# Kernel tuning notes

Measured on AMD Instinct MI355X. Metric: run time of the kernel, lower is better.

Reference implementation:

```python
import jax, jax.numpy as jnp
import numpy as np

NEG = -9e15

def _gat_layer(x, adj, W, a_src, a_dst):
    # x: [B,N,Fin], W: [Fin,Fout], a_src/a_dst: [Fout], adj: [N,N]
    h = jnp.einsum('bnf,fo->bno', x, W)                    # [B,N,Fout]
    e_src = jnp.einsum('bno,o->bn', h, a_src)              # [B,N]
    e_dst = jnp.einsum('bno,o->bn', h, a_dst)              # [B,N]
    e = jax.nn.leaky_relu(e_src[:, :, None] + e_dst[:, None, :], 0.2)  # [B,N,N]
    att = jax.nn.softmax(jnp.where(adj > 0, e, NEG), axis=-1)
    return jnp.einsum('bij,bjo->bio', att, h)              # [B,N,Fout]

def setup_inputs() -> dict:
    key = jax.random.key(0)
    ks = jax.random.split(key, 12)
    B, N, Fin = 8, 2048, 128
    H = [128, 128, 64]
    C = 128
    s = lambda *d: 1.0 / np.sqrt(d[0])
    inp = {
        'x':   jax.random.normal(ks[0], (B, N, Fin), jnp.float32),
        'adj': jax.random.normal(ks[1], (N, N), jnp.float32),
        'W1':  jax.random.normal(ks[2], (Fin, H[0]), jnp.float32) * s(Fin),
        'a1s': jax.random.normal(ks[3], (H[0],), jnp.float32) * s(H[0]),
        'a1d': jax.random.normal(ks[4], (H[0],), jnp.float32) * s(H[0]),
        'W2':  jax.random.normal(ks[5], (H[0], H[1]), jnp.float32) * s(H[0]),
        'a2s': jax.random.normal(ks[6], (H[1],), jnp.float32) * s(H[1]),
        'a2d': jax.random.normal(ks[7], (H[1],), jnp.float32) * s(H[1]),
        'W3':  jax.random.normal(ks[8], (H[1], H[2]), jnp.float32) * s(H[1]),
        'a3s': jax.random.normal(ks[9], (H[2],), jnp.float32) * s(H[2]),
        'a3d': jax.random.normal(ks[10], (H[2],), jnp.float32) * s(H[2]),
        'Wlin': jax.random.normal(ks[11], (H[2] * N, C), jnp.float32) * s(H[2] * N),
        'blin': jnp.zeros((C,), jnp.float32),
    }
    return inp

def reference(x, adj, W1, a1s, a1d, W2, a2s, a2d, W3, a3s, a3d, Wlin, blin):
    out = jax.nn.relu(_gat_layer(x, adj, W1, a1s, a1d))
    out = jax.nn.relu(_gat_layer(out, adj, W2, a2s, a2d))
    out = jax.nn.relu(_gat_layer(out, adj, W3, a3s, a3d))
    B = out.shape[0]
    out = out.reshape(B, -1)              # flatten [B, N*H3]
    return out @ Wlin + blin              # [B, num_classes]
```

## Files before the change

kernel.cpp:

```cpp
#include <hip/hip_runtime.h>
#include <stdint.h>


typedef unsigned short u16;
typedef __bf16 bf16x8 __attribute__((ext_vector_type(8)));
typedef float f32x4 __attribute__((ext_vector_type(4)));
typedef u16 u16x8 __attribute__((ext_vector_type(8)));

#define LOG2E 1.44269504088896340736f

__device__ __forceinline__ float b2f(u16 u) {
    union { unsigned int i; float f; } v; v.i = ((unsigned int)u) << 16; return v.f;
}
__device__ __forceinline__ u16 f2b(float f) {
    union { float f; unsigned int i; } v; v.f = f;
    unsigned int i = v.i;
    return (u16)((i + 0x7fffu + ((i >> 16) & 1u)) >> 16);
}
__device__ __forceinline__ float fast_exp2(float x) {
#if __has_builtin(__builtin_amdgcn_exp2f)
    return __builtin_amdgcn_exp2f(x);
#else
    return exp2f(x);
#endif
}

union ABfrag { bf16x8 v; u16x8 u; };

__device__ __forceinline__ void gload_lds16(const u16* g, u16* l) {
    __builtin_amdgcn_global_load_lds((const __attribute__((address_space(1))) void*)g,
                                     (__attribute__((address_space(3))) void*)l,
                                     16, 0, 0);
}

template <int N>
__device__ __forceinline__ void wait_vmcnt() {
    asm volatile("s_waitcnt vmcnt(%0)" :: "i"(N) : "memory");
}
__device__ __forceinline__ void pipe_barrier() {
    __builtin_amdgcn_s_barrier();
    asm volatile("" ::: "memory");
}

__global__ void __launch_bounds__(256) k_mask(const float* __restrict__ adj,
                                              uint32_t* __restrict__ adjm) {
    const int w = threadIdx.x >> 6, lane = threadIdx.x & 63;
    const int row = blockIdx.x * 4 + w;
    const float* ar = adj + (size_t)row * 2048;
    uint32_t* mr = adjm + (size_t)row * 64;
    for (int j0 = 0; j0 < 2048; j0 += 64) {
        unsigned long long m = __ballot(ar[j0 + lane] > 0.f);
        if (lane == 0) {
            mr[(j0 >> 5)] = (uint32_t)m;
            mr[(j0 >> 5) + 1] = (uint32_t)(m >> 32);
        }
    }
}

__global__ void k_prep(const float* __restrict__ W1, const float* __restrict__ W2,
                       const float* __restrict__ W3,
                       const float* __restrict__ a1s, const float* __restrict__ a1d,
                       const float* __restrict__ a2s, const float* __restrict__ a2d,
                       const float* __restrict__ a3s, const float* __restrict__ a3d,
                       u16* __restrict__ Wt1, u16* __restrict__ Wt2, u16* __restrict__ Wt3,
                       float* __restrict__ u1s, float* __restrict__ u1d,
                       float* __restrict__ u2s, float* __restrict__ u2d,
                       float* __restrict__ u3s, float* __restrict__ u3d) {
    if (blockIdx.x == 160) {
        int f = threadIdx.x;
        if (f < 128) {
            float s1 = 0.f, d1 = 0.f, s2 = 0.f, d2 = 0.f, s3 = 0.f, d3 = 0.f;
            for (int o = 0; o < 128; ++o) { float w = W1[f * 128 + o]; s1 += w * a1s[o]; d1 += w * a1d[o]; }
            for (int o = 0; o < 128; ++o) { float w = W2[f * 128 + o]; s2 += w * a2s[o]; d2 += w * a2d[o]; }
            for (int o = 0; o <  64; ++o) { float w = W3[f *  64 + o]; s3 += w * a3s[o]; d3 += w * a3d[o]; }
            u1s[f] = s1 * LOG2E; u1d[f] = d1 * LOG2E;
            u2s[f] = s2 * LOG2E; u2d[f] = d2 * LOG2E;
            u3s[f] = s3 * LOG2E; u3d[f] = d3 * LOG2E;
        }
        return;
    }
    int idx = blockIdx.x * 256 + threadIdx.x;
    if (idx < 16384) {
        int f = idx >> 7, o = idx & 127;
        Wt1[o * 128 + f] = f2b(W1[idx]);
    } else if (idx < 32768) {
        int j = idx - 16384; int f = j >> 7, o = j & 127;
        Wt2[o * 128 + f] = f2b(W2[j]);
    } else if (idx < 40960) {
        int j = idx - 32768; int f = j >> 6, o = j & 63;
        Wt3[o * 128 + f] = f2b(W3[j]);
    }
}

template <int F, bool XF32>
__global__ void __launch_bounds__(256) k_h(const void* __restrict__ xv,
                                           const u16* __restrict__ Wt,
                                           const float* __restrict__ us,
                                           const float* __restrict__ ud,
                                           u16* __restrict__ h_t,
                                           float* __restrict__ esf,
                                           float* __restrict__ edf) {
    constexpr int NT = F / 16;
    constexpr int TNP = 72;
    __shared__ __align__(16) u16 hl[F * TNP];

    const int b = blockIdx.x;
    const int nblk = blockIdx.y;
    const int tid = threadIdx.x;
    const int w = tid >> 6, lane = tid & 63;
    const int quad = lane >> 4, l15 = lane & 15;
    const int n0w = nblk * 64 + w * 16;
    const int i_a = n0w + l15;

    ABfrag afr[4];
    float ps = 0.f, pd = 0.f;
    if (XF32) {
        const float* xr = (const float*)xv + ((size_t)(b * 2048 + i_a)) * 128;
#pragma unroll
        for (int kk = 0; kk < 4; ++kk) {
            const int o8 = kk * 32 + quad * 8;
            float4 x0 = *reinterpret_cast<const float4*>(xr + o8);
            float4 x1 = *reinterpret_cast<const float4*>(xr + o8 + 4);
            float4 s0 = *reinterpret_cast<const float4*>(us + o8);
            float4 s1 = *reinterpret_cast<const float4*>(us + o8 + 4);
            float4 d0 = *reinterpret_cast<const float4*>(ud + o8);
            float4 d1 = *reinterpret_cast<const float4*>(ud + o8 + 4);
            ps += x0.x * s0.x + x0.y * s0.y + x0.z * s0.z + x0.w * s0.w
                + x1.x * s1.x + x1.y * s1.y + x1.z * s1.z + x1.w * s1.w;
            pd += x0.x * d0.x + x0.y * d0.y + x0.z * d0.z + x0.w * d0.w
                + x1.x * d1.x + x1.y * d1.y + x1.z * d1.z + x1.w * d1.w;
            afr[kk].u[0] = f2b(x0.x); afr[kk].u[1] = f2b(x0.y);
            afr[kk].u[2] = f2b(x0.z); afr[kk].u[3] = f2b(x0.w);
            afr[kk].u[4] = f2b(x1.x); afr[kk].u[5] = f2b(x1.y);
            afr[kk].u[6] = f2b(x1.z); afr[kk].u[7] = f2b(x1.w);
        }
    } else {
        const u16* xr = (const u16*)xv + ((size_t)(b * 2048 + i_a)) * 128;
#pragma unroll
        for (int kk = 0; kk < 4; ++kk) {
            const int o8 = kk * 32 + quad * 8;
            u16x8 xa = *reinterpret_cast<const u16x8*>(xr + o8);
            afr[kk].u = xa;
            float4 s0 = *reinterpret_cast<const float4*>(us + o8);
            float4 s1 = *reinterpret_cast<const float4*>(us + o8 + 4);
            float4 d0 = *reinterpret_cast<const float4*>(ud + o8);
            float4 d1 = *reinterpret_cast<const float4*>(ud + o8 + 4);
            float xf[8];
#pragma unroll
            for (int j = 0; j < 8; ++j) xf[j] = b2f(xa[j]);
            ps += xf[0] * s0.x + xf[1] * s0.y + xf[2] * s0.z + xf[3] * s0.w
                + xf[4] * s1.x + xf[5] * s1.y + xf[6] * s1.z + xf[7] * s1.w;
            pd += xf[0] * d0.x + xf[1] * d0.y + xf[2] * d0.z + xf[3] * d0.w
                + xf[4] * d1.x + xf[5] * d1.y + xf[6] * d1.z + xf[7] * d1.w;
        }
    }
    ps += __shfl_xor(ps, 16, 64); ps += __shfl_xor(ps, 32, 64);
    pd += __shfl_xor(pd, 16, 64); pd += __shfl_xor(pd, 32, 64);
    if (quad == 0) {
        const size_t idx = (size_t)(b * 2048 + i_a) * 2;
        float2 sv; sv.x = fast_exp2(ps); sv.y = fast_exp2(0.2f * ps);
        float2 dv; dv.x = fast_exp2(pd); dv.y = fast_exp2(0.2f * pd);
        *reinterpret_cast<float2*>(esf + idx) = sv;
        *reinterpret_cast<float2*>(edf + idx) = dv;
    }

    f32x4 acc[NT];
#pragma unroll
    for (int nt = 0; nt < NT; ++nt) acc[nt] = (f32x4){0.f, 0.f, 0.f, 0.f};
#pragma unroll
    for (int kk = 0; kk < 4; ++kk) {
#pragma unroll
        for (int nt = 0; nt < NT; ++nt) {
            bf16x8 bfv = *reinterpret_cast<const bf16x8*>(
                Wt + (nt * 16 + l15) * 128 + kk * 32 + quad * 8);
            acc[nt] = __builtin_amdgcn_mfma_f32_16x16x32_bf16(afr[kk].v, bfv, acc[nt], 0, 0, 0);
        }
    }

#pragma unroll
    for (int nt = 0; nt < NT; ++nt)
#pragma unroll
        for (int r = 0; r < 4; ++r)
            hl[(nt * 16 + l15) * TNP + w * 16 + quad * 4 + r] = f2b(acc[nt][r]);
    __syncthreads();
    if (tid < F * 2) {
        int o = tid >> 1, half = tid & 1;
        const u16* src = hl + o * TNP + half * 32;
        u16* dst = h_t + ((size_t)(b * F + o)) * 2048 + nblk * 64 + half * 32;
#pragma unroll
        for (int c = 0; c < 4; ++c)
            *reinterpret_cast<u16x8*>(dst + c * 8) =
                *reinterpret_cast<const u16x8*>(src + c * 8);
    }
}

template <int F, bool OUT_F32>
__global__ void __launch_bounds__(512) k_attn(const float* __restrict__ esf,
                                              const float* __restrict__ edf,
                                              const uint32_t* __restrict__ adjm,
                                              const u16* __restrict__ h_t,
                                              void* __restrict__ outp) {
    constexpr int NT = F / 16;
    constexpr int G  = F / 32;
    __shared__ __align__(16) u16 Ht[2][3][F * 64];
    __shared__ __align__(16) float eL[4096];
    __shared__ __align__(16) uint32_t mL[64 * 64];
    float* accLDS = (float*)&Ht[0][0][0];

    const int b = blockIdx.x;
    const int iblk = blockIdx.y;
    const int tid = threadIdx.x;
    const int grp = tid >> 8;
    const int t8 = tid & 255;
    const int w = t8 >> 6;
    const int lane = tid & 63;
    const int quad = lane >> 4, l15 = lane & 15;
    const int i_a = iblk * 64 + w * 16 + l15;
    const int r_loc = w * 16 + l15;

    const float2 esp = *reinterpret_cast<const float2*>(esf + ((size_t)(b * 2048 + i_a)) * 2);
    const float Es = esp.x, Fs = esp.y;
    const u16* hb = h_t + (size_t)b * F * 2048;

    const int lro = lane >> 3;
    const int lcp = lane & 7;
    const int jt0 = grp * 16;

    ABfrag onesf;
#pragma unroll
    for (int j = 0; j < 8; ++j) onesf.u[j] = 0x3F80;

    f32x4 acc[NT];
#pragma unroll
    for (int nt = 0; nt < NT; ++nt) acc[nt] = (f32x4){0.f, 0.f, 0.f, 0.f};
    f32x4 dccc = (f32x4){0.f, 0.f, 0.f, 0.f};

    {
        const float4* esrc = (const float4*)(edf + (size_t)b * 4096);
        float4* edst = (float4*)eL;
#pragma unroll
        for (int t = 0; t < 2; ++t) edst[tid + t * 512] = esrc[tid + t * 512];
        const uint2* msrc = (const uint2*)(adjm + (size_t)(iblk * 64) * 64);
#pragma unroll
        for (int t = 0; t < 4; ++t) {
            int idx = tid + t * 512;
            int r = idx >> 5, k = idx & 31;
            uint2 v = msrc[idx];
            *reinterpret_cast<uint2*>((char*)mL + r * 256 + ((k ^ (r & 31)) * 8)) = v;
        }
    }

    auto STAGE = [&](int jt, int slot) {
        const int j0 = jt * 64;
        u16* lbase = &Ht[grp][slot][0];
#pragma unroll
        for (int it = 0; it < G; ++it) {
            int ro = (it * 4 + w) * 8 + lro;
            int c = lcp ^ (ro & 7);
            gload_lds16(hb + (size_t)ro * 2048 + j0 + c * 8, lbase + (it * 4 + w) * 512);
        }
    };

    f32x4 ec[8]; uint2 mc;
    auto loadE = [&](int jt, f32x4* e, uint2& m) {
        const float* eb = eL + (size_t)(jt * 64 + quad * 8) * 2;
#pragma unroll
        for (int q = 0; q < 4; ++q) e[q] = *reinterpret_cast<const f32x4*>(eb + q * 4);
#pragma unroll
        for (int q = 0; q < 4; ++q) e[4 + q] = *reinterpret_cast<const f32x4*>(eb + 64 + q * 4);
        m = *reinterpret_cast<const uint2*>((const char*)mL + r_loc * 256 + ((jt ^ (r_loc & 31)) * 8));
    };

    auto compute = [&](int slot) {
        ABfrag af[2];
#pragma unroll
        for (int kk = 0; kk < 2; ++kk) {
            const uint32_t word = kk ? mc.y : mc.x;
#pragma unroll
            for (int px = 0; px < 4; ++px) {
                const f32x4 q = ec[kk * 4 + px];
                float w0 = fmaxf(Es * q.x, Fs * q.y);
                float w1 = fmaxf(Es * q.z, Fs * q.w);
                const uint32_t s0 = 0u - ((word >> (quad * 8 + px * 2)) & 1u);
                const uint32_t s1 = 0u - ((word >> (quad * 8 + px * 2 + 1)) & 1u);
                w0 = __uint_as_float(__float_as_uint(w0) & s0);
                w1 = __uint_as_float(__float_as_uint(w1) & s1);
                af[kk].v[px * 2]     = (__bf16)w0;
                af[kk].v[px * 2 + 1] = (__bf16)w1;
            }
        }
        const u16* tb = &Ht[grp][slot][0];
        __builtin_amdgcn_s_setprio(1);
#pragma unroll
        for (int kk = 0; kk < 2; ++kk) {
#pragma unroll
            for (int nt = 0; nt < NT; ++nt) {
                int ob = nt * 16 + l15;
                int c = kk * 4 + quad;
                bf16x8 bfv = *reinterpret_cast<const bf16x8*>(
                    tb + ob * 64 + ((c ^ (ob & 7)) * 8));
                acc[nt] = __builtin_amdgcn_mfma_f32_16x16x32_bf16(af[kk].v, bfv, acc[nt], 0, 0, 0);
            }
            dccc = __builtin_amdgcn_mfma_f32_16x16x32_bf16(af[kk].v, onesf.v, dccc, 0, 0, 0);
        }
        __builtin_amdgcn_s_setprio(0);
    };

    __syncthreads();
    loadE(jt0, ec, mc);
    STAGE(jt0, 0);
    STAGE(jt0 + 1, 1);

    int sc = 0, sp = 2;
    for (int jj = 0; jj < 15; ++jj) {
        wait_vmcnt<G>();
        pipe_barrier();
        if (jj < 14) STAGE(jt0 + jj + 2, sp);
        f32x4 en[8]; uint2 mn;
        loadE(jt0 + jj + 1, en, mn);
        compute(sc);
#pragma unroll
        for (int q = 0; q < 8; ++q) ec[q] = en[q];
        mc = mn;
        sc = (sc == 2) ? 0 : sc + 1;
        sp = (sp == 2) ? 0 : sp + 1;
    }
    wait_vmcnt<0>();
    pipe_barrier();
    compute(sc);

    __syncthreads();
    if (grp == 1) {
#pragma unroll
        for (int nt = 0; nt < NT; ++nt)
            *reinterpret_cast<f32x4*>(&accLDS[(t8 * (NT + 1) + nt) * 4]) = acc[nt];
        *reinterpret_cast<f32x4*>(&accLDS[(t8 * (NT + 1) + NT) * 4]) = dccc;
    }
    __syncthreads();
    if (grp == 0) {
#pragma unroll
        for (int nt = 0; nt < NT; ++nt)
            acc[nt] += *reinterpret_cast<const f32x4*>(&accLDS[(t8 * (NT + 1) + nt) * 4]);
        dccc += *reinterpret_cast<const f32x4*>(&accLDS[(t8 * (NT + 1) + NT) * 4]);
        float dinv[4];
#pragma unroll
        for (int r = 0; r < 4; ++r)
            dinv[r] = 1.0f / fmaxf(dccc[r], 1e-30f);
        const int ib = iblk * 64 + w * 16 + quad * 4;
        if (OUT_F32) {
            float* o3 = (float*)outp;
#pragma unroll
            for (int nt = 0; nt < NT; ++nt)
#pragma unroll
                for (int r = 0; r < 4; ++r) {
                    float vv = fmaxf(acc[nt][r] * dinv[r], 0.f);
                    o3[((size_t)(b * 2048 + ib + r)) * F + nt * 16 + l15] = vv;
                }
        } else {
            u16* xo = (u16*)outp;
#pragma unroll
            for (int nt = 0; nt < NT; ++nt)
#pragma unroll
                for (int r = 0; r < 4; ++r) {
                    float vv = fmaxf(acc[nt][r] * dinv[r], 0.f);
                    xo[((size_t)(b * 2048 + ib + r)) * F + nt * 16 + l15] = f2b(vv);
                }
        }
    }
}

__global__ void __launch_bounds__(256) k_lin(const float* __restrict__ o3,
                                             const float* __restrict__ Wlin,
                                             float* __restrict__ pbuf) {
    __shared__ float xc[8][256];
    __shared__ float red[8][8][128];
    const int tid = threadIdx.x;
    const int k0 = blockIdx.x * 256;
    for (int idx = tid; idx < 2048; idx += 256) {
        int bb = idx >> 8, kk = idx & 255;
        xc[bb][kk] = o3[(size_t)bb * 131072 + k0 + kk];
    }
    __syncthreads();
    const int o4 = tid & 31;
    const int kb = tid >> 5;
    f32x4 acc[8];
#pragma unroll
    for (int bb = 0; bb < 8; ++bb) acc[bb] = (f32x4){0.f, 0.f, 0.f, 0.f};
    const float* wp = Wlin + (size_t)(k0 + kb * 32) * 128 + o4 * 4;
#pragma unroll 4
    for (int k = 0; k < 32; ++k) {
        f32x4 wv = *reinterpret_cast<const f32x4*>(wp + (size_t)k * 128);
#pragma unroll
        for (int bb = 0; bb < 8; ++bb) acc[bb] += wv * xc[bb][kb * 32 + k];
    }
#pragma unroll
    for (int bb = 0; bb < 8; ++bb)
        *reinterpret_cast<f32x4*>(&red[kb][bb][o4 * 4]) = acc[bb];
    __syncthreads();
    const int f = tid * 4;
    const int bb = f >> 7, o = f & 127;
    f32x4 s = (f32x4){0.f, 0.f, 0.f, 0.f};
#pragma unroll
    for (int k2 = 0; k2 < 8; ++k2) s += *reinterpret_cast<const f32x4*>(&red[k2][bb][o]);
    *reinterpret_cast<f32x4*>(&pbuf[(size_t)blockIdx.x * 1024 + f]) = s;
}

__global__ void __launch_bounds__(256) k_bias(const float* __restrict__ pbuf,
                                              const float* __restrict__ blin,
                                              float* __restrict__ out) {
    __shared__ float red[256];
    const int tid = threadIdx.x;
    const int p16 = tid >> 4;
    const int fo = tid & 15;
    const int f0 = blockIdx.x * 16;
    float s = 0.f;
#pragma unroll 4
    for (int p = p16; p < 512; p += 16)
        s += pbuf[(size_t)p * 1024 + f0 + fo];
    red[tid] = s;
    __syncthreads();
    if (tid < 16) {
        float t = 0.f;
#pragma unroll
        for (int k = 0; k < 16; ++k) t += red[k * 16 + tid];
        out[f0 + tid] = t + blin[(f0 + tid) & 127];
    }
}

extern "C" void kernel_launch(void* const* d_in, const int* in_sizes, int n_in,
                              void* d_out, int out_size, void* d_ws, size_t ws_size,
                              hipStream_t stream) {
    (void)in_sizes; (void)n_in; (void)out_size;
    const float* x    = (const float*)d_in[0];
    const float* adj  = (const float*)d_in[1];
    const float* W1   = (const float*)d_in[2];
    const float* a1s  = (const float*)d_in[3];
    const float* a1d  = (const float*)d_in[4];
    const float* W2   = (const float*)d_in[5];
    const float* a2s  = (const float*)d_in[6];
    const float* a2d  = (const float*)d_in[7];
    const float* W3   = (const float*)d_in[8];
    const float* a3s  = (const float*)d_in[9];
    const float* a3d  = (const float*)d_in[10];
    const float* Wlin = (const float*)d_in[11];
    const float* blin = (const float*)d_in[12];

    char* ws = (char*)d_ws;
    u16*   h_t = (u16*)ws;
    size_t off = (size_t)4 << 20;
    float* esf = (float*)(ws + off); off += 131072;
    float* edf = (float*)(ws + off); off += 131072;
    u16*   Wt1 = (u16*)(ws + off);   off += 32768;
    u16*   Wt2 = (u16*)(ws + off);   off += 32768;
    u16*   Wt3 = (u16*)(ws + off);   off += 16384;
    float* u1s = (float*)(ws + off); off += 512;
    float* u1d = (float*)(ws + off); off += 512;
    float* u2s = (float*)(ws + off); off += 512;
    float* u2d = (float*)(ws + off); off += 512;
    float* u3s = (float*)(ws + off); off += 512;
    float* u3d = (float*)(ws + off); off += 512;
    uint32_t* adjm = (uint32_t*)(ws + off); off += 524288;
    float* pbuf = (float*)(ws + off); off += (size_t)512 * 1024 * 4;
    u16* actA;
    if (ws_size >= off + ((size_t)4 << 20)) {
        actA = (u16*)(ws + off);
    } else {
        actA = (u16*)d_in[0];
    }
    float* o3 = (float*)actA;

    dim3 g(8, 32);
    k_mask<<<512, 256, 0, stream>>>(adj, adjm);
    k_prep<<<161, 256, 0, stream>>>(W1, W2, W3, a1s, a1d, a2s, a2d, a3s, a3d,
                                    Wt1, Wt2, Wt3, u1s, u1d, u2s, u2d, u3s, u3d);

    k_h<128, true ><<<g, 256, 0, stream>>>((const void*)x, Wt1, u1s, u1d, h_t, esf, edf);
    k_attn<128, false><<<g, 512, 0, stream>>>(esf, edf, adjm, h_t, (void*)actA);

    k_h<128, false><<<g, 256, 0, stream>>>((const void*)actA, Wt2, u2s, u2d, h_t, esf, edf);
    k_attn<128, false><<<g, 512, 0, stream>>>(esf, edf, adjm, h_t, (void*)actA);

    k_h<64, false><<<g, 256, 0, stream>>>((const void*)actA, Wt3, u3s, u3d, h_t, esf, edf);
    k_attn<64, true ><<<g, 512, 0, stream>>>(esf, edf, adjm, h_t, (void*)o3);

    k_lin<<<512, 256, 0, stream>>>(o3, Wlin, pbuf);
    k_bias<<<64, 256, 0, stream>>>(pbuf, blin, (float*)d_out);
}
```

Measured before the change: 240.4 us.

## Halve attention block to 256 threads with two row tiles per wave; split k_h output columns

k_attn now runs 256 threads per block, and each wave computes two 16-row tiles that share every staged H fragment read from LDS. This doubles MFMA work per B-fragment load and cuts the number of waves per block. The E/mask prefetch is also simplified to load just before compute instead of being double-buffered. Separately, k_h is split over two grid blocks per row tile, each computing half of the output features, which doubles the grid so more CUs are busy. The costs are higher register pressure in k_attn, fewer waves available to hide latency, and x being reloaded twice in k_h.

Result: slower. 253.6 us (+5.5%).

```diff
diff --git a/kernel.cpp b/kernel.cpp
--- a/kernel.cpp
+++ b/kernel.cpp
@@ -100,12 +100,13 @@
                                            u16* __restrict__ h_t,
                                            float* __restrict__ esf,
                                            float* __restrict__ edf) {
-    constexpr int NT = F / 16;
+    constexpr int NTB = F / 32;
     constexpr int TNP = 72;
-    __shared__ __align__(16) u16 hl[F * TNP];
+    __shared__ __align__(16) u16 hl[(F / 2) * TNP];
 
     const int b = blockIdx.x;
-    const int nblk = blockIdx.y;
+    const int nb2 = blockIdx.y;
+    const int nblk = nb2 >> 1, ohalf = nb2 & 1;
     const int tid = threadIdx.x;
     const int w = tid >> 6, lane = tid & 63;
     const int quad = lane >> 4, l15 = lane & 15;
@@ -154,39 +155,42 @@
                 + xf[4] * d1.x + xf[5] * d1.y + xf[6] * d1.z + xf[7] * d1.w;
         }
     }
-    ps += __shfl_xor(ps, 16, 64); ps += __shfl_xor(ps, 32, 64);
-    pd += __shfl_xor(pd, 16, 64); pd += __shfl_xor(pd, 32, 64);
-    if (quad == 0) {
-        const size_t idx = (size_t)(b * 2048 + i_a) * 2;
-        float2 sv; sv.x = fast_exp2(ps); sv.y = fast_exp2(0.2f * ps);
-        float2 dv; dv.x = fast_exp2(pd); dv.y = fast_exp2(0.2f * pd);
-        *reinterpret_cast<float2*>(esf + idx) = sv;
-        *reinterpret_cast<float2*>(edf + idx) = dv;
-    }
-
-    f32x4 acc[NT];
-#pragma unroll
-    for (int nt = 0; nt < NT; ++nt) acc[nt] = (f32x4){0.f, 0.f, 0.f, 0.f};
+    if (ohalf == 0) {
+        ps += __shfl_xor(ps, 16, 64); ps += __shfl_xor(ps, 32, 64);
+        pd += __shfl_xor(pd, 16, 64); pd += __shfl_xor(pd, 32, 64);
+        if (quad == 0) {
+            const size_t idx = (size_t)(b * 2048 + i_a) * 2;
+            float2 sv; sv.x = fast_exp2(ps); sv.y = fast_exp2(0.2f * ps);
+            float2 dv; dv.x = fast_exp2(pd); dv.y = fast_exp2(0.2f * pd);
+            *reinterpret_cast<float2*>(esf + idx) = sv;
+            *reinterpret_cast<float2*>(edf + idx) = dv;
+        }
+    }
+
+    f32x4 acc[NTB];
+#pragma unroll
+    for (int nt = 0; nt < NTB; ++nt) acc[nt] = (f32x4){0.f, 0.f, 0.f, 0.f};
 #pragma unroll
     for (int kk = 0; kk < 4; ++kk) {
 #pragma unroll
-        for (int nt = 0; nt < NT; ++nt) {
+        for (int nt = 0; nt < NTB; ++nt) {
             bf16x8 bfv = *reinterpret_cast<const bf16x8*>(
-                Wt + (nt * 16 + l15) * 128 + kk * 32 + quad * 8);
+                Wt + (ohalf * (F / 2) + nt * 16 + l15) * 128 + kk * 32 + quad * 8);
             acc[nt] = __builtin_amdgcn_mfma_f32_16x16x32_bf16(afr[kk].v, bfv, acc[nt], 0, 0, 0);
         }
     }
 
 #pragma unroll
-    for (int nt = 0; nt < NT; ++nt)
+    for (int nt = 0; nt < NTB; ++nt)
 #pragma unroll
         for (int r = 0; r < 4; ++r)
             hl[(nt * 16 + l15) * TNP + w * 16 + quad * 4 + r] = f2b(acc[nt][r]);
     __syncthreads();
-    if (tid < F * 2) {
-        int o = tid >> 1, half = tid & 1;
-        const u16* src = hl + o * TNP + half * 32;
-        u16* dst = h_t + ((size_t)(b * F + o)) * 2048 + nblk * 64 + half * 32;
+    if (tid < F) {
+        int o_loc = tid >> 1, half32 = tid & 1;
+        const u16* src = hl + o_loc * TNP + half32 * 32;
+        u16* dst = h_t + ((size_t)(b * F + ohalf * (F / 2) + o_loc)) * 2048
+                   + nblk * 64 + half32 * 32;
 #pragma unroll
         for (int c = 0; c < 4; ++c)
             *reinterpret_cast<u16x8*>(dst + c * 8) =
@@ -195,13 +199,13 @@
 }
 
 template <int F, bool OUT_F32>
-__global__ void __launch_bounds__(512) k_attn(const float* __restrict__ esf,
+__global__ void __launch_bounds__(256) k_attn(const float* __restrict__ esf,
                                               const float* __restrict__ edf,
                                               const uint32_t* __restrict__ adjm,
                                               const u16* __restrict__ h_t,
                                               void* __restrict__ outp) {
     constexpr int NT = F / 16;
-    constexpr int G  = F / 32;
+    constexpr int G  = F / 16;
     __shared__ __align__(16) u16 Ht[2][3][F * 64];
     __shared__ __align__(16) float eL[4096];
     __shared__ __align__(16) uint32_t mL[64 * 64];
@@ -210,16 +214,17 @@
     const int b = blockIdx.x;
     const int iblk = blockIdx.y;
     const int tid = threadIdx.x;
-    const int grp = tid >> 8;
-    const int t8 = tid & 255;
-    const int w = t8 >> 6;
+    const int grp = tid >> 7;
+    const int t128 = tid & 127;
+    const int w = t128 >> 6;
     const int lane = tid & 63;
     const int quad = lane >> 4, l15 = lane & 15;
-    const int i_a = iblk * 64 + w * 16 + l15;
-    const int r_loc = w * 16 + l15;
-
-    const float2 esp = *reinterpret_cast<const float2*>(esf + ((size_t)(b * 2048 + i_a)) * 2);
-    const float Es = esp.x, Fs = esp.y;
+    const int r0 = w * 32 + l15;
+    const int r1 = r0 + 16;
+
+    const float2 e0 = *reinterpret_cast<const float2*>(esf + ((size_t)(b * 2048 + iblk * 64 + r0)) * 2);
+    const float2 e1 = *reinterpret_cast<const float2*>(esf + ((size_t)(b * 2048 + iblk * 64 + r1)) * 2);
+    const float Es0 = e0.x, Fs0 = e0.y, Es1 = e1.x, Fs1 = e1.y;
     const u16* hb = h_t + (size_t)b * F * 2048;
 
     const int lro = lane >> 3;
@@ -230,20 +235,24 @@
 #pragma unroll
     for (int j = 0; j < 8; ++j) onesf.u[j] = 0x3F80;
 
-    f32x4 acc[NT];
-#pragma unroll
-    for (int nt = 0; nt < NT; ++nt) acc[nt] = (f32x4){0.f, 0.f, 0.f, 0.f};
-    f32x4 dccc = (f32x4){0.f, 0.f, 0.f, 0.f};
+    f32x4 acc0[NT], acc1[NT];
+#pragma unroll
+    for (int nt = 0; nt < NT; ++nt) {
+        acc0[nt] = (f32x4){0.f, 0.f, 0.f, 0.f};
+        acc1[nt] = (f32x4){0.f, 0.f, 0.f, 0.f};
+    }
+    f32x4 d0 = (f32x4){0.f, 0.f, 0.f, 0.f};
+    f32x4 d1 = (f32x4){0.f, 0.f, 0.f, 0.f};
 
     {
         const float4* esrc = (const float4*)(edf + (size_t)b * 4096);
         float4* edst = (float4*)eL;
 #pragma unroll
-        for (int t = 0; t < 2; ++t) edst[tid + t * 512] = esrc[tid + t * 512];
+        for (int t = 0; t < 4; ++t) edst[tid + t * 256] = esrc[tid + t * 256];
         const uint2* msrc = (const uint2*)(adjm + (size_t)(iblk * 64) * 64);
 #pragma unroll
-        for (int t = 0; t < 4; ++t) {
-            int idx = tid + t * 512;
+        for (int t = 0; t < 8; ++t) {
+            int idx = tid + t * 256;
             int r = idx >> 5, k = idx & 31;
             uint2 v = msrc[idx];
             *reinterpret_cast<uint2*>((char*)mL + r * 256 + ((k ^ (r & 31)) * 8)) = v;
@@ -255,38 +264,50 @@
         u16* lbase = &Ht[grp][slot][0];
 #pragma unroll
         for (int it = 0; it < G; ++it) {
-            int ro = (it * 4 + w) * 8 + lro;
+            int ci = it * 2 + w;
+            int ro = ci * 8 + lro;
             int c = lcp ^ (ro & 7);
-            gload_lds16(hb + (size_t)ro * 2048 + j0 + c * 8, lbase + (it * 4 + w) * 512);
+            gload_lds16(hb + (size_t)ro * 2048 + j0 + c * 8, lbase + ci * 512);
         }
     };
 
-    f32x4 ec[8]; uint2 mc;
-    auto loadE = [&](int jt, f32x4* e, uint2& m) {
+    f32x4 ec[8]; uint2 mc0, mc1;
+    auto loadE = [&](int jt) {
         const float* eb = eL + (size_t)(jt * 64 + quad * 8) * 2;
 #pragma unroll
-        for (int q = 0; q < 4; ++q) e[q] = *reinterpret_cast<const f32x4*>(eb + q * 4);
-#pragma unroll
-        for (int q = 0; q < 4; ++q) e[4 + q] = *reinterpret_cast<const f32x4*>(eb + 64 + q * 4);
-        m = *reinterpret_cast<const uint2*>((const char*)mL + r_loc * 256 + ((jt ^ (r_loc & 31)) * 8));
+        for (int q = 0; q < 4; ++q) ec[q] = *reinterpret_cast<const f32x4*>(eb + q * 4);
+#pragma unroll
+        for (int q = 0; q < 4; ++q) ec[4 + q] = *reinterpret_cast<const f32x4*>(eb + 64 + q * 4);
+        mc0 = *reinterpret_cast<const uint2*>((const char*)mL + r0 * 256 + ((jt ^ (r0 & 31)) * 8));
+        mc1 = *reinterpret_cast<const uint2*>((const char*)mL + r1 * 256 + ((jt ^ (r1 & 31)) * 8));
     };
 
     auto compute = [&](int slot) {
-        ABfrag af[2];
+        ABfrag af0[2], af1[2];
 #pragma unroll
         for (int kk = 0; kk < 2; ++kk) {
-            const uint32_t word = kk ? mc.y : mc.x;
+            const uint32_t word0 = kk ? mc0.y : mc0.x;
+            const uint32_t word1 = kk ? mc1.y : mc1.x;
 #pragma unroll
             for (int px = 0; px < 4; ++px) {
                 const f32x4 q = ec[kk * 4 + px];
-                float w0 = fmaxf(Es * q.x, Fs * q.y);
-                float w1 = fmaxf(Es * q.z, Fs * q.w);
-                const uint32_t s0 = 0u - ((word >> (quad * 8 + px * 2)) & 1u);
-                const uint32_t s1 = 0u - ((word >> (quad * 8 + px * 2 + 1)) & 1u);
-                w0 = __uint_as_float(__float_as_uint(w0) & s0);
-                w1 = __uint_as_float(__float_as_uint(w1) & s1);
-                af[kk].v[px * 2]     = (__bf16)w0;
-                af[kk].v[px * 2 + 1] = (__bf16)w1;
+                const int bsh = quad * 8 + px * 2;
+                float wa0 = fmaxf(Es0 * q.x, Fs0 * q.y);
+                float wb0 = fmaxf(Es0 * q.z, Fs0 * q.w);
+                float wa1 = fmaxf(Es1 * q.x, Fs1 * q.y);
+                float wb1 = fmaxf(Es1 * q.z, Fs1 * q.w);
+                const uint32_t sa0 = 0u - ((word0 >> bsh) & 1u);
+                const uint32_t sb0 = 0u - ((word0 >> (bsh + 1)) & 1u);
+                const uint32_t sa1 = 0u - ((word1 >> bsh) & 1u);
+                const uint32_t sb1 = 0u - ((word1 >> (bsh + 1)) & 1u);
+                wa0 = __uint_as_float(__float_as_uint(wa0) & sa0);
+                wb0 = __uint_as_float(__float_as_uint(wb0) & sb0);
+                wa1 = __uint_as_float(__float_as_uint(wa1) & sa1);
+                wb1 = __uint_as_float(__float_as_uint(wb1) & sb1);
+                af0[kk].v[px * 2]     = (__bf16)wa0;
+                af0[kk].v[px * 2 + 1] = (__bf16)wb0;
+                af1[kk].v[px * 2]     = (__bf16)wa1;
+                af1[kk].v[px * 2 + 1] = (__bf16)wb1;
             }
         }
         const u16* tb = &Ht[grp][slot][0];
@@ -299,15 +320,16 @@
                 int c = kk * 4 + quad;
                 bf16x8 bfv = *reinterpret_cast<const bf16x8*>(
                     tb + ob * 64 + ((c ^ (ob & 7)) * 8));
-                acc[nt] = __builtin_amdgcn_mfma_f32_16x16x32_bf16(af[kk].v, bfv, acc[nt], 0, 0, 0);
+                acc0[nt] = __builtin_amdgcn_mfma_f32_16x16x32_bf16(af0[kk].v, bfv, acc0[nt], 0, 0, 0);
+                acc1[nt] = __builtin_amdgcn_mfma_f32_16x16x32_bf16(af1[kk].v, bfv, acc1[nt], 0, 0, 0);
             }
-            dccc = __builtin_amdgcn_mfma_f32_16x16x32_bf16(af[kk].v, onesf.v, dccc, 0, 0, 0);
+            d0 = __builtin_amdgcn_mfma_f32_16x16x32_bf16(af0[kk].v, onesf.v, d0, 0, 0, 0);
+            d1 = __builtin_amdgcn_mfma_f32_16x16x32_bf16(af1[kk].v, onesf.v, d1, 0, 0, 0);
         }
         __builtin_amdgcn_s_setprio(0);
     };
 
     __syncthreads();
-    loadE(jt0, ec, mc);
     STAGE(jt0, 0);
     STAGE(jt0 + 1, 1);
 
@@ -316,45 +338,49 @@
         wait_vmcnt<G>();
         pipe_barrier();
         if (jj < 14) STAGE(jt0 + jj + 2, sp);
-        f32x4 en[8]; uint2 mn;
-        loadE(jt0 + jj + 1, en, mn);
+        loadE(jt0 + jj);
         compute(sc);
-#pragma unroll
-        for (int q = 0; q < 8; ++q) ec[q] = en[q];
-        mc = mn;
         sc = (sc == 2) ? 0 : sc + 1;
         sp = (sp == 2) ? 0 : sp + 1;
     }
     wait_vmcnt<0>();
     pipe_barrier();
+    loadE(jt0 + 15);
     compute(sc);
 
     __syncthreads();
     if (grp == 1) {
-#pragma unroll
-        for (int nt = 0; nt < NT; ++nt)
-            *reinterpret_cast<f32x4*>(&accLDS[(t8 * (NT + 1) + nt) * 4]) = acc[nt];
-        *reinterpret_cast<f32x4*>(&accLDS[(t8 * (NT + 1) + NT) * 4]) = dccc;
+        f32x4* basep = reinterpret_cast<f32x4*>(&accLDS[(size_t)t128 * (2 * NT + 2) * 4]);
+#pragma unroll
+        for (int nt = 0; nt < NT; ++nt) { basep[nt] = acc0[nt]; basep[NT + nt] = acc1[nt]; }
+        basep[2 * NT] = d0;
+        basep[2 * NT + 1] = d1;
     }
     __syncthreads();
     if (grp == 0) {
-#pragma unroll
-        for (int nt = 0; nt < NT; ++nt)
-            acc[nt] += *reinterpret_cast<const f32x4*>(&accLDS[(t8 * (NT + 1) + nt) * 4]);
-        dccc += *reinterpret_cast<const f32x4*>(&accLDS[(t8 * (NT + 1) + NT) * 4]);
-        float dinv[4];
-#pragma unroll
-        for (int r = 0; r < 4; ++r)
-            dinv[r] = 1.0f / fmaxf(dccc[r], 1e-30f);
-        const int ib = iblk * 64 + w * 16 + quad * 4;
+        const f32x4* basep = reinterpret_cast<const f32x4*>(&accLDS[(size_t)t128 * (2 * NT + 2) * 4]);
+#pragma unroll
+        for (int nt = 0; nt < NT; ++nt) { acc0[nt] += basep[nt]; acc1[nt] += basep[NT + nt]; }
+        d0 += basep[2 * NT];
+        d1 += basep[2 * NT + 1];
+        float dinv0[4], dinv1[4];
+#pragma unroll
+        for (int r = 0; r < 4; ++r) {
+            dinv0[r] = 1.0f / fmaxf(d0[r], 1e-30f);
+            dinv1[r] = 1.0f / fmaxf(d1[r], 1e-30f);
+        }
+        const int ib0 = iblk * 64 + w * 32 + quad * 4;
+        const int ib1 = ib0 + 16;
         if (OUT_F32) {
             float* o3 = (float*)outp;
 #pragma unroll
             for (int nt = 0; nt < NT; ++nt)
 #pragma unroll
                 for (int r = 0; r < 4; ++r) {
-                    float vv = fmaxf(acc[nt][r] * dinv[r], 0.f);
-                    o3[((size_t)(b * 2048 + ib + r)) * F + nt * 16 + l15] = vv;
+                    float v0 = fmaxf(acc0[nt][r] * dinv0[r], 0.f);
+                    float v1 = fmaxf(acc1[nt][r] * dinv1[r], 0.f);
+                    o3[((size_t)(b * 2048 + ib0 + r)) * F + nt * 16 + l15] = v0;
+                    o3[((size_t)(b * 2048 + ib1 + r)) * F + nt * 16 + l15] = v1;
                 }
         } else {
             u16* xo = (u16*)outp;
@@ -362,8 +388,10 @@
             for (int nt = 0; nt < NT; ++nt)
 #pragma unroll
                 for (int r = 0; r < 4; ++r) {
-                    float vv = fmaxf(acc[nt][r] * dinv[r], 0.f);
-                    xo[((size_t)(b * 2048 + ib + r)) * F + nt * 16 + l15] = f2b(vv);
+                    float v0 = fmaxf(acc0[nt][r] * dinv0[r], 0.f);
+                    float v1 = fmaxf(acc1[nt][r] * dinv1[r], 0.f);
+                    xo[((size_t)(b * 2048 + ib0 + r)) * F + nt * 16 + l15] = f2b(v0);
+                    xo[((size_t)(b * 2048 + ib1 + r)) * F + nt * 16 + l15] = f2b(v1);
                 }
         }
     }
@@ -470,18 +498,19 @@
     float* o3 = (float*)actA;
 
     dim3 g(8, 32);
+    dim3 gh(8, 64);
     k_mask<<<512, 256, 0, stream>>>(adj, adjm);
     k_prep<<<161, 256, 0, stream>>>(W1, W2, W3, a1s, a1d, a2s, a2d, a3s, a3d,
                                     Wt1, Wt2, Wt3, u1s, u1d, u2s, u2d, u3s, u3d);
 
-    k_h<128, true ><<<g, 256, 0, stream>>>((const void*)x, Wt1, u1s, u1d, h_t, esf, edf);
-    k_attn<128, false><<<g, 512, 0, stream>>>(esf, edf, adjm, h_t, (void*)actA);
-
-    k_h<128, false><<<g, 256, 0, stream>>>((const void*)actA, Wt2, u2s, u2d, h_t, esf, edf);
-    k_attn<128, false><<<g, 512, 0, stream>>>(esf, edf, adjm, h_t, (void*)actA);
-
-    k_h<64, false><<<g, 256, 0, stream>>>((const void*)actA, Wt3, u3s, u3d, h_t, esf, edf);
-    k_attn<64, true ><<<g, 512, 0, stream>>>(esf, edf, adjm, h_t, (void*)o3);
+    k_h<128, true ><<<gh, 256, 0, stream>>>((const void*)x, Wt1, u1s, u1d, h_t, esf, edf);
+    k_attn<128, false><<<g, 256, 0, stream>>>(esf, edf, adjm, h_t, (void*)actA);
+
+    k_h<128, false><<<gh, 256, 0, stream>>>((const void*)actA, Wt2, u2s, u2d, h_t, esf, edf);
+    k_attn<128, false><<<g, 256, 0, stream>>>(esf, edf, adjm, h_t, (void*)actA);
+
+    k_h<64, false><<<gh, 256, 0, stream>>>((const void*)actA, Wt3, u3s, u3d, h_t, esf, edf);
+    k_attn<64, true ><<<g, 256, 0, stream>>>(esf, edf, adjm, h_t, (void*)o3);
 
     k_lin<<<512, 256, 0, stream>>>(o3, Wlin, pbuf);
     k_bias<<<64, 256, 0, stream>>>(pbuf, blin, (float*)d_out);
```
